# Performance work log

Measured on AMD Instinct MI355X. Metric: run time of the kernel, lower is better.

## Reference

```python
import jax, jax.numpy as jnp
import numpy as np

NUM_HEADS = 16


def setup_inputs() -> dict:
    key = jax.random.key(0)
    k1, k2, k3, k4, k5 = jax.random.split(key, 5)
    B, N, E = 16, 8, 2048
    H = NUM_HEADS
    D = E // H
    KV = 4096
    return {
        "x": jax.random.normal(k1, (B, N, E), dtype=jnp.float32),
        "past_k": jax.random.normal(k2, (B, H, KV, D), dtype=jnp.float32),
        "past_v": jax.random.normal(k3, (B, H, KV, D), dtype=jnp.float32),
        "W_qkv": jax.random.normal(k4, (3 * E, E), dtype=jnp.float32) * (E ** -0.5),
        "W_out": jax.random.normal(k5, (E, E), dtype=jnp.float32) * (E ** -0.5),
    }


def reference(x, past_k, past_v, W_qkv, W_out):
    B, N, E = x.shape
    H = NUM_HEADS
    D = E // H
    # fused QKV projection: [B, N, 3E]
    qkv = jnp.einsum("bne,fe->bnf", x, W_qkv)
    q, k_new, v_new = jnp.split(qkv, 3, axis=-1)
    # '... n (h d) -> ... h n d'
    to_heads = lambda t: t.reshape(B, N, H, D).swapaxes(1, 2)
    q, k_new, v_new = to_heads(q), to_heads(k_new), to_heads(v_new)
    # KV cache append along seq dim
    k = jnp.concatenate([past_k, k_new], axis=-2)  # [B, H, KV+N, D]
    v = jnp.concatenate([past_v, v_new], axis=-2)
    # SDPA (eval mode -> is_causal=False)
    scale = D ** -0.5
    scores = jnp.einsum("bhqd,bhkd->bhqk", q, k) * scale
    attn = jax.nn.softmax(scores, axis=-1)
    out = jnp.einsum("bhqk,bhkd->bhqd", attn, v)  # [B, H, N, D]
    # '... h n d -> ... n (h d)'
    out = out.swapaxes(1, 2).reshape(B, N, E)
    out = jnp.einsum("bne,fe->bnf", out, W_out)
    return (out, k, v)
```

## Files before the change

### kernel.cpp

```cpp
#include <hip/hip_runtime.h>
#include <cstddef>
#include <cstdint>

#define B_ 16
#define H_ 16
#define NQ 8
#define D_ 128
#define E_ 2048
#define F3 6144
#define KVP 4096
#define KVT 4104
#define SCALE 0.08838834764831843f
#define NCHUNK 8
#define CHUNK 512
#define SUBR 32
#define NSUB 16
#define PARTSZ 1040

typedef float f32x4_t __attribute__((ext_vector_type(4)));

__device__ __forceinline__ void nt_store4(float* p, float4 v) {
  f32x4_t w;
  w.x = v.x; w.y = v.y; w.z = v.z; w.w = v.w;
  __builtin_nontemporal_store(w, reinterpret_cast<f32x4_t*>(p));
}

template <int BM, int BN, int SPLITK>
__global__ __launch_bounds__(256) void gemm_xwt(const float* __restrict__ X,
                                                const float* __restrict__ W,
                                                float* __restrict__ C,
                                                int K, int Fdim) {
  constexpr int BK = 32;
  constexpr int RM = BM / 16;
  constexpr int RN = BN / 16;
  __shared__ float xs[BK][BM + 4];
  __shared__ float wss[BK][BN + 4];
  const int t = threadIdx.x;
  const int tm = t >> 4, tn = t & 15;
  const int m0 = blockIdx.y * BM, f0 = blockIdx.x * BN;
  const int kbeg = (SPLITK > 1) ? blockIdx.z * (K / SPLITK) : 0;
  const int kend = (SPLITK > 1) ? kbeg + K / SPLITK : K;
  if (SPLITK > 1) C += (size_t)blockIdx.z * 128 * Fdim;
  float acc[RM][RN];
#pragma unroll
  for (int i = 0; i < RM; ++i)
#pragma unroll
    for (int j = 0; j < RN; ++j) acc[i][j] = 0.f;

  for (int kk = kbeg; kk < kend; kk += BK) {
#pragma unroll
    for (int i = 0; i < (BM * BK) / 1024; ++i) {
      int j = t + i * 256;
      int r = j >> 3;
      int c = (j & 7) << 2;
      float4 v = *reinterpret_cast<const float4*>(&X[(size_t)(m0 + r) * K + kk + c]);
      xs[c + 0][r] = v.x; xs[c + 1][r] = v.y; xs[c + 2][r] = v.z; xs[c + 3][r] = v.w;
    }
#pragma unroll
    for (int i = 0; i < (BN * BK) / 1024; ++i) {
      int j = t + i * 256;
      int r = j >> 3;
      int c = (j & 7) << 2;
      float4 v = *reinterpret_cast<const float4*>(&W[(size_t)(f0 + r) * K + kk + c]);
      wss[c + 0][r] = v.x; wss[c + 1][r] = v.y; wss[c + 2][r] = v.z; wss[c + 3][r] = v.w;
    }
    __syncthreads();
#pragma unroll
    for (int k = 0; k < BK; ++k) {
      float xv[RM], wv[RN];
      if constexpr (RM == 4) {
        *reinterpret_cast<float4*>(xv) = *reinterpret_cast<const float4*>(&xs[k][tm * 4]);
      } else {
        *reinterpret_cast<float2*>(xv) = *reinterpret_cast<const float2*>(&xs[k][tm * 2]);
      }
      if constexpr (RN == 4) {
        *reinterpret_cast<float4*>(wv) = *reinterpret_cast<const float4*>(&wss[k][tn * 4]);
      } else {
        *reinterpret_cast<float2*>(wv) = *reinterpret_cast<const float2*>(&wss[k][tn * 2]);
      }
#pragma unroll
      for (int i = 0; i < RM; ++i)
#pragma unroll
        for (int j = 0; j < RN; ++j) acc[i][j] += xv[i] * wv[j];
    }
    __syncthreads();
  }
#pragma unroll
  for (int i = 0; i < RM; ++i) {
    float* cp = &C[(size_t)(m0 + tm * RM + i) * Fdim + f0 + tn * RN];
    if constexpr (RN == 4) {
      *reinterpret_cast<float4*>(cp) = make_float4(acc[i][0], acc[i][1], acc[i][2], acc[i][3]);
    } else {
      *reinterpret_cast<float2*>(cp) = make_float2(acc[i][0], acc[i][1]);
    }
  }
}

__global__ __launch_bounds__(256) void add2(const float* __restrict__ a,
                                            const float* __restrict__ b,
                                            float* __restrict__ o) {
  int i = blockIdx.x * 256 + threadIdx.x;
  float4 va = reinterpret_cast<const float4*>(a)[i];
  float4 vb = reinterpret_cast<const float4*>(b)[i];
  reinterpret_cast<float4*>(o)[i] =
      make_float4(va.x + vb.x, va.y + vb.y, va.z + vb.z, va.w + vb.w);
}

__global__ __launch_bounds__(256) void attn_partial(
    const float* __restrict__ past_k, const float* __restrict__ past_v,
    const float* __restrict__ qkv_a, const float* __restrict__ qkv_b,
    float* __restrict__ out_k, float* __restrict__ out_v,
    float* __restrict__ part) {
  const int t = threadIdx.x;
  const int c = blockIdx.x, h = blockIdx.y, b = blockIdx.z;
  const int bh = b * H_ + h;
  const int g = t & 31, rg = t >> 5;

  __shared__ float red[4096];
  __shared__ float f_lds[NQ];
  __shared__ float m_lds[2][NQ], l_lds[2][NQ];
  float* s_lds = red;
  float* p_lds = red + 288;

  float4 qreg[NQ];
#pragma unroll
  for (int qi = 0; qi < NQ; ++qi) {
    const size_t qoff = (size_t)(b * NQ + qi) * F3 + h * D_ + g * 4;
    float4 q0 = *reinterpret_cast<const float4*>(&qkv_a[qoff]);
    if (qkv_b) {
      float4 q1 = *reinterpret_cast<const float4*>(&qkv_b[qoff]);
      q0.x += q1.x; q0.y += q1.y; q0.z += q1.z; q0.w += q1.w;
    }
    qreg[qi] = q0;
  }

  if (t < NQ) { m_lds[0][t] = -1e30f; l_lds[0][t] = 0.f; }

  const float* gk = past_k + ((size_t)bh * KVP + (size_t)c * CHUNK) * D_;
  const float* gv = past_v + ((size_t)bh * KVP + (size_t)c * CHUNK) * D_;
  float* ok = out_k + ((size_t)bh * KVT + (size_t)c * CHUNK) * D_;
  float* ov = out_v + ((size_t)bh * KVT + (size_t)c * CHUNK) * D_;

  float4 acc[NQ];
#pragma unroll
  for (int qi = 0; qi < NQ; ++qi) acc[qi] = make_float4(0.f, 0.f, 0.f, 0.f);

  const int b0 = g & 1, b1 = (g >> 1) & 1, b2 = (g >> 2) & 1;
  const int qsel = 4 * b0 + 2 * b1 + b2;

  auto loadf = [&](float4 (&kf)[4], float4 (&vf)[4], int sub) {
    const size_t off = (size_t)sub * SUBR * D_;
#pragma unroll
    for (int i = 0; i < 4; ++i) {
      const size_t ga = off + (size_t)(rg + 8 * i) * D_ + g * 4;
      kf[i] = *reinterpret_cast<const float4*>(&gk[ga]);
      vf[i] = *reinterpret_cast<const float4*>(&gv[ga]);
    }
  };

  auto bodyf = [&](float4 (&kf)[4], float4 (&vf)[4], float4 (&kfN)[4],
                   float4 (&vfN)[4], int sub, bool pf) {
    const int cur = sub & 1, nxt = cur ^ 1;
    const size_t off = (size_t)sub * SUBR * D_;
#pragma unroll
    for (int i = 0; i < 4; ++i) {
      const int r = rg + 8 * i;
      const size_t ga = off + (size_t)r * D_ + g * 4;
      nt_store4(&ok[ga], kf[i]);
      nt_store4(&ov[ga], vf[i]);
      float sp[NQ];
#pragma unroll
      for (int qi = 0; qi < NQ; ++qi)
        sp[qi] = kf[i].x * qreg[qi].x + kf[i].y * qreg[qi].y +
                 kf[i].z * qreg[qi].z + kf[i].w * qreg[qi].w;
      float v1[4];
#pragma unroll
      for (int j = 0; j < 4; ++j) {
        float x = b0 ? sp[j] : sp[j + 4];
        v1[j] = (b0 ? sp[j + 4] : sp[j]) + __shfl_xor(x, 1);
      }
      float v2[2];
#pragma unroll
      for (int j = 0; j < 2; ++j) {
        float x = b1 ? v1[j] : v1[j + 2];
        v2[j] = (b1 ? v1[j + 2] : v1[j]) + __shfl_xor(x, 2);
      }
      float v3;
      {
        float x = b2 ? v2[0] : v2[1];
        v3 = (b2 ? v2[1] : v2[0]) + __shfl_xor(x, 4);
      }
      v3 += __shfl_xor(v3, 8);
      v3 += __shfl_xor(v3, 16);
      if (g < 8) s_lds[r * 9 + qsel] = v3;
    }
    __syncthreads();

    {
      const int srow = t & 31, sqi = t >> 5;
      float s = s_lds[srow * 9 + sqi] * SCALE;
      float cmax = s;
#pragma unroll
      for (int o = 16; o > 0; o >>= 1) cmax = fmaxf(cmax, __shfl_xor(cmax, o));
      float mo = m_lds[cur][sqi];
      float mn = fmaxf(mo, cmax);
      float p = __expf(s - mn);
      float psum = p;
#pragma unroll
      for (int o = 16; o > 0; o >>= 1) psum += __shfl_xor(psum, o);
      p_lds[srow * 8 + sqi] = p;
      if (srow == 0) {
        float f = __expf(mo - mn);
        f_lds[sqi] = f;
        m_lds[nxt][sqi] = mn;
        l_lds[nxt][sqi] = l_lds[cur][sqi] * f + psum;
      }
    }
    __syncthreads();

    if (pf) loadf(kfN, vfN, sub + 1);

    {
      float4 f0 = *reinterpret_cast<const float4*>(&f_lds[0]);
      float4 f1 = *reinterpret_cast<const float4*>(&f_lds[4]);
      acc[0].x *= f0.x; acc[0].y *= f0.x; acc[0].z *= f0.x; acc[0].w *= f0.x;
      acc[1].x *= f0.y; acc[1].y *= f0.y; acc[1].z *= f0.y; acc[1].w *= f0.y;
      acc[2].x *= f0.z; acc[2].y *= f0.z; acc[2].z *= f0.z; acc[2].w *= f0.z;
      acc[3].x *= f0.w; acc[3].y *= f0.w; acc[3].z *= f0.w; acc[3].w *= f0.w;
      acc[4].x *= f1.x; acc[4].y *= f1.x; acc[4].z *= f1.x; acc[4].w *= f1.x;
      acc[5].x *= f1.y; acc[5].y *= f1.y; acc[5].z *= f1.y; acc[5].w *= f1.y;
      acc[6].x *= f1.z; acc[6].y *= f1.z; acc[6].z *= f1.z; acc[6].w *= f1.z;
      acc[7].x *= f1.w; acc[7].y *= f1.w; acc[7].z *= f1.w; acc[7].w *= f1.w;
#pragma unroll
      for (int i = 0; i < 4; ++i) {
        const int r = rg + 8 * i;
        float4 pa = *reinterpret_cast<const float4*>(&p_lds[r * 8]);
        float4 pc = *reinterpret_cast<const float4*>(&p_lds[r * 8 + 4]);
        acc[0].x += pa.x * vf[i].x; acc[0].y += pa.x * vf[i].y; acc[0].z += pa.x * vf[i].z; acc[0].w += pa.x * vf[i].w;
        acc[1].x += pa.y * vf[i].x; acc[1].y += pa.y * vf[i].y; acc[1].z += pa.y * vf[i].z; acc[1].w += pa.y * vf[i].w;
        acc[2].x += pa.z * vf[i].x; acc[2].y += pa.z * vf[i].y; acc[2].z += pa.z * vf[i].z; acc[2].w += pa.z * vf[i].w;
        acc[3].x += pa.w * vf[i].x; acc[3].y += pa.w * vf[i].y; acc[3].z += pa.w * vf[i].z; acc[3].w += pa.w * vf[i].w;
        acc[4].x += pc.x * vf[i].x; acc[4].y += pc.x * vf[i].y; acc[4].z += pc.x * vf[i].z; acc[4].w += pc.x * vf[i].w;
        acc[5].x += pc.y * vf[i].x; acc[5].y += pc.y * vf[i].y; acc[5].z += pc.y * vf[i].z; acc[5].w += pc.y * vf[i].w;
        acc[6].x += pc.z * vf[i].x; acc[6].y += pc.z * vf[i].y; acc[6].z += pc.z * vf[i].z; acc[6].w += pc.z * vf[i].w;
        acc[7].x += pc.w * vf[i].x; acc[7].y += pc.w * vf[i].y; acc[7].z += pc.w * vf[i].z; acc[7].w += pc.w * vf[i].w;
      }
    }
  };

  __syncthreads();

  float4 kfA[4], vfA[4], kfB[4], vfB[4];
  loadf(kfA, vfA, 0);
  for (int sub = 0; sub < NSUB; sub += 2) {
    bodyf(kfA, vfA, kfB, vfB, sub, true);
    bodyf(kfB, vfB, kfA, vfA, sub + 1, sub + 2 < NSUB);
  }

  __syncthreads();

#pragma unroll
  for (int half = 4; half >= 1; half >>= 1) {
    if (rg >= half && rg < 2 * half) {
#pragma unroll
      for (int qi = 0; qi < NQ; ++qi)
        *reinterpret_cast<float4*>(&red[(rg - half) * 1024 + qi * 128 + g * 4]) = acc[qi];
    }
    __syncthreads();
    if (rg < half) {
#pragma unroll
      for (int qi = 0; qi < NQ; ++qi) {
        float4 o = *reinterpret_cast<const float4*>(&red[rg * 1024 + qi * 128 + g * 4]);
        acc[qi].x += o.x; acc[qi].y += o.y; acc[qi].z += o.z; acc[qi].w += o.w;
      }
    }
    __syncthreads();
  }

  float* pb = part + ((size_t)bh * NCHUNK + c) * PARTSZ;
  if (t < NQ) { pb[t] = m_lds[0][t]; pb[8 + t] = l_lds[0][t]; }
  if (rg == 0) {
#pragma unroll
    for (int qi = 0; qi < NQ; ++qi)
      *reinterpret_cast<float4*>(&pb[16 + qi * 128 + g * 4]) = acc[qi];
  }
}

__global__ __launch_bounds__(256) void attn_combine(
    const float* __restrict__ qkv_a, const float* __restrict__ qkv_b,
    const float* __restrict__ part, float* __restrict__ out_k,
    float* __restrict__ out_v, float* __restrict__ attn) {
  const int t = threadIdx.x;
  const int h = blockIdx.x, b = blockIdx.y;
  const int bh = b * H_ + h;
  __shared__ float q_lds[NQ * 132];
  __shared__ float kn_lds[NQ * 132];
  __shared__ float vn_lds[NQ * 132];
  __shared__ float p9[NQ * 12];
  __shared__ float m9_lds[NQ], s9_lds[NQ];
  {
    int n = t >> 5, g = t & 31;
    const size_t soff = (size_t)(b * NQ + n) * F3 + h * D_ + g * 4;
    float4 qv = *reinterpret_cast<const float4*>(&qkv_a[soff]);
    float4 kv = *reinterpret_cast<const float4*>(&qkv_a[soff + E_]);
    float4 vv = *reinterpret_cast<const float4*>(&qkv_a[soff + 2 * E_]);
    if (qkv_b) {
      float4 q1 = *reinterpret_cast<const float4*>(&qkv_b[soff]);
      float4 k1 = *reinterpret_cast<const float4*>(&qkv_b[soff + E_]);
      float4 v1 = *reinterpret_cast<const float4*>(&qkv_b[soff + 2 * E_]);
      qv.x += q1.x; qv.y += q1.y; qv.z += q1.z; qv.w += q1.w;
      kv.x += k1.x; kv.y += k1.y; kv.z += k1.z; kv.w += k1.w;
      vv.x += v1.x; vv.y += v1.y; vv.z += v1.z; vv.w += v1.w;
    }
    *reinterpret_cast<float4*>(&q_lds[n * 132 + g * 4]) = qv;
    *reinterpret_cast<float4*>(&kn_lds[n * 132 + g * 4]) = kv;
    *reinterpret_cast<float4*>(&vn_lds[n * 132 + g * 4]) = vv;
    *reinterpret_cast<float4*>(&out_k[((size_t)bh * KVT + KVP + n) * D_ + g * 4]) = kv;
    *reinterpret_cast<float4*>(&out_v[((size_t)bh * KVT + KVP + n) * D_ + g * 4]) = vv;
  }
  __syncthreads();
  if (t < 64) {
    int nq = t >> 3, nk = t & 7;
    float s = 0.f;
#pragma unroll
    for (int g = 0; g < 32; ++g) {
      float4 qv = *reinterpret_cast<const float4*>(&q_lds[nq * 132 + g * 4]);
      float4 kv = *reinterpret_cast<const float4*>(&kn_lds[nk * 132 + g * 4]);
      s += qv.x * kv.x + qv.y * kv.y + qv.z * kv.z + qv.w * kv.w;
    }
    s *= SCALE;
    float mx = s;
#pragma unroll
    for (int o = 4; o > 0; o >>= 1) mx = fmaxf(mx, __shfl_xor(mx, o));
    float p = __expf(s - mx);
    float sm = p;
#pragma unroll
    for (int o = 4; o > 0; o >>= 1) sm += __shfl_xor(sm, o);
    p9[nk * 12 + nq] = p;
    if (nk == 0) { m9_lds[nq] = mx; s9_lds[nq] = sm; }
  }
  __syncthreads();
  const int qg = t >> 7, dcol = t & 127;
  const float* pb = part + (size_t)bh * NCHUNK * PARTSZ;
#pragma unroll
  for (int jq = 0; jq < 4; ++jq) {
    int qi = qg * 4 + jq;
    float M = m9_lds[qi];
#pragma unroll
    for (int c = 0; c < NCHUNK; ++c) M = fmaxf(M, pb[(size_t)c * PARTSZ + qi]);
    float num = 0.f, den = 0.f;
#pragma unroll
    for (int c = 0; c < NCHUNK; ++c) {
      const float* pc = pb + (size_t)c * PARTSZ;
      float wgt = __expf(pc[qi] - M);
      den += wgt * pc[8 + qi];
      num += wgt * pc[16 + (size_t)qi * D_ + dcol];
    }
    float acc9 = 0.f;
#pragma unroll
    for (int r = 0; r < NQ; ++r) acc9 += p9[r * 12 + qi] * vn_lds[r * 132 + dcol];
    float w9 = __expf(m9_lds[qi] - M);
    num += w9 * acc9;
    den += w9 * s9_lds[qi];
    attn[((size_t)(b * NQ + qi)) * E_ + h * D_ + dcol] = num / den;
  }
}

extern "C" void kernel_launch(void* const* d_in, const int* in_sizes, int n_in,
                              void* d_out, int out_size, void* d_ws, size_t ws_size,
                              hipStream_t stream) {
  const float* x      = (const float*)d_in[0];
  const float* past_k = (const float*)d_in[1];
  const float* past_v = (const float*)d_in[2];
  const float* W_qkv  = (const float*)d_in[3];
  const float* W_out  = (const float*)d_in[4];

  float* out   = (float*)d_out;
  float* out_k = out + (size_t)B_ * NQ * E_;
  float* out_v = out_k + (size_t)B_ * H_ * KVT * D_;

  const size_t QKV_N  = (size_t)B_ * NQ * F3;
  const size_t PART_N = (size_t)B_ * H_ * NCHUNK * PARTSZ;
  const size_t ATTN_N = (size_t)B_ * NQ * E_;
  const size_t need2  = (2 * QKV_N + PART_N + 3 * ATTN_N) * sizeof(float);

  float* ws = (float*)d_ws;
  const bool split2 = ws_size >= need2;

  float* pq0  = ws;
  float* pq1  = split2 ? ws + QKV_N : nullptr;
  float* part = ws + (split2 ? 2 : 1) * QKV_N;
  float* attn = part + PART_N;
  float* po0  = attn + ATTN_N;

  if (split2) {
    gemm_xwt<64, 64, 2><<<dim3(F3 / 64, 2, 2), 256, 0, stream>>>(x, W_qkv, pq0, E_, F3);
  } else {
    gemm_xwt<64, 64, 1><<<dim3(F3 / 64, 2), 256, 0, stream>>>(x, W_qkv, pq0, E_, F3);
  }
  attn_partial<<<dim3(NCHUNK, H_, B_), 256, 0, stream>>>(past_k, past_v, pq0, pq1,
                                                         out_k, out_v, part);
  attn_combine<<<dim3(H_, B_), 256, 0, stream>>>(pq0, pq1, part, out_k, out_v, attn);
  if (split2) {
    gemm_xwt<64, 64, 2><<<dim3(E_ / 64, 2, 2), 256, 0, stream>>>(attn, W_out, po0, E_, E_);
    add2<<<dim3(ATTN_N / 1024), 256, 0, stream>>>(po0, po0 + ATTN_N, out);
  } else {
    gemm_xwt<64, 64, 1><<<dim3(E_ / 64, 2), 256, 0, stream>>>(attn, W_out, out, E_, E_);
  }
}
```

Before: 568.0 us.

## Give each wave its own KV slice with wave-local online softmax

Restructures attn_partial so each of the 4 waves owns 128 contiguous KV rows and keeps its own running max and sum in registers. Per-wave LDS scratch with an lgkmcnt fence replaces the block-wide __syncthreads barriers. The waves' partial results are merged at the end with a log-sum-exp rescale. Non-temporal stores become ordinary stores, and K/V prefetch is issued one step earlier. The cost is a more complex final combine and reliance on intra-wave LDS ordering without a barrier.

```diff
diff --git a/kernel.cpp b/kernel.cpp
--- a/kernel.cpp
+++ b/kernel.cpp
@@ -13,17 +13,9 @@
 #define SCALE 0.08838834764831843f
 #define NCHUNK 8
 #define CHUNK 512
-#define SUBR 32
-#define NSUB 16
 #define PARTSZ 1040
 
-typedef float f32x4_t __attribute__((ext_vector_type(4)));
-
-__device__ __forceinline__ void nt_store4(float* p, float4 v) {
-  f32x4_t w;
-  w.x = v.x; w.y = v.y; w.z = v.z; w.w = v.w;
-  __builtin_nontemporal_store(w, reinterpret_cast<f32x4_t*>(p));
-}
+#define WAVE_LDS_FENCE() asm volatile("s_waitcnt lgkmcnt(0)" ::: "memory")
 
 template <int BM, int BN, int SPLITK>
 __global__ __launch_bounds__(256) void gemm_xwt(const float* __restrict__ X,
@@ -114,13 +106,15 @@
   const int t = threadIdx.x;
   const int c = blockIdx.x, h = blockIdx.y, b = blockIdx.z;
   const int bh = b * H_ + h;
-  const int g = t & 31, rg = t >> 5;
+  const int l = t & 63, w = t >> 6;
+  const int g = l & 31, half = l >> 5;
 
   __shared__ float red[4096];
-  __shared__ float f_lds[NQ];
-  __shared__ float m_lds[2][NQ], l_lds[2][NQ];
-  float* s_lds = red;
-  float* p_lds = red + 288;
+  __shared__ float scratch[4][160];
+  __shared__ float mw_lds[32], lw_lds[32];
+  float* s_w = scratch[w];
+  float* p_w = scratch[w] + 72;
+  float* f_w = scratch[w] + 136;
 
   float4 qreg[NQ];
 #pragma unroll
@@ -134,8 +128,7 @@
     qreg[qi] = q0;
   }
 
-  if (t < NQ) { m_lds[0][t] = -1e30f; l_lds[0][t] = 0.f; }
-
+  const int wbase = w * 128;
   const float* gk = past_k + ((size_t)bh * KVP + (size_t)c * CHUNK) * D_;
   const float* gv = past_v + ((size_t)bh * KVP + (size_t)c * CHUNK) * D_;
   float* ok = out_k + ((size_t)bh * KVT + (size_t)c * CHUNK) * D_;
@@ -144,46 +137,44 @@
   float4 acc[NQ];
 #pragma unroll
   for (int qi = 0; qi < NQ; ++qi) acc[qi] = make_float4(0.f, 0.f, 0.f, 0.f);
+  float m_run = -1e30f, l_run = 0.f;
 
   const int b0 = g & 1, b1 = (g >> 1) & 1, b2 = (g >> 2) & 1;
   const int qsel = 4 * b0 + 2 * b1 + b2;
-
-  auto loadf = [&](float4 (&kf)[4], float4 (&vf)[4], int sub) {
-    const size_t off = (size_t)sub * SUBR * D_;
-#pragma unroll
-    for (int i = 0; i < 4; ++i) {
-      const size_t ga = off + (size_t)(rg + 8 * i) * D_ + g * 4;
-      kf[i] = *reinterpret_cast<const float4*>(&gk[ga]);
-      vf[i] = *reinterpret_cast<const float4*>(&gv[ga]);
+  const int srow = l & 7, sqi = l >> 3;
+
+  auto loadf = [&](float4 (&kf)[4], float4 (&vf)[4], int it) {
+#pragma unroll
+    for (int j = 0; j < 4; ++j) {
+      const size_t ga = (size_t)(wbase + it * 8 + half + 2 * j) * D_ + g * 4;
+      kf[j] = *reinterpret_cast<const float4*>(&gk[ga]);
+      vf[j] = *reinterpret_cast<const float4*>(&gv[ga]);
     }
   };
 
-  auto bodyf = [&](float4 (&kf)[4], float4 (&vf)[4], float4 (&kfN)[4],
-                   float4 (&vfN)[4], int sub, bool pf) {
-    const int cur = sub & 1, nxt = cur ^ 1;
-    const size_t off = (size_t)sub * SUBR * D_;
-#pragma unroll
-    for (int i = 0; i < 4; ++i) {
-      const int r = rg + 8 * i;
-      const size_t ga = off + (size_t)r * D_ + g * 4;
-      nt_store4(&ok[ga], kf[i]);
-      nt_store4(&ov[ga], vf[i]);
+  auto bodyf = [&](float4 (&kf)[4], float4 (&vf)[4], int it) {
+#pragma unroll
+    for (int j = 0; j < 4; ++j) {
+      const int r = half + 2 * j;
+      const size_t ga = (size_t)(wbase + it * 8 + r) * D_ + g * 4;
+      *reinterpret_cast<float4*>(&ok[ga]) = kf[j];
+      *reinterpret_cast<float4*>(&ov[ga]) = vf[j];
       float sp[NQ];
 #pragma unroll
       for (int qi = 0; qi < NQ; ++qi)
-        sp[qi] = kf[i].x * qreg[qi].x + kf[i].y * qreg[qi].y +
-                 kf[i].z * qreg[qi].z + kf[i].w * qreg[qi].w;
+        sp[qi] = kf[j].x * qreg[qi].x + kf[j].y * qreg[qi].y +
+                 kf[j].z * qreg[qi].z + kf[j].w * qreg[qi].w;
       float v1[4];
 #pragma unroll
-      for (int j = 0; j < 4; ++j) {
-        float x = b0 ? sp[j] : sp[j + 4];
-        v1[j] = (b0 ? sp[j + 4] : sp[j]) + __shfl_xor(x, 1);
+      for (int jj = 0; jj < 4; ++jj) {
+        float x = b0 ? sp[jj] : sp[jj + 4];
+        v1[jj] = (b0 ? sp[jj + 4] : sp[jj]) + __shfl_xor(x, 1);
       }
       float v2[2];
 #pragma unroll
-      for (int j = 0; j < 2; ++j) {
-        float x = b1 ? v1[j] : v1[j + 2];
-        v2[j] = (b1 ? v1[j + 2] : v1[j]) + __shfl_xor(x, 2);
+      for (int jj = 0; jj < 2; ++jj) {
+        float x = b1 ? v1[jj] : v1[jj + 2];
+        v2[jj] = (b1 ? v1[jj + 2] : v1[jj]) + __shfl_xor(x, 2);
       }
       float v3;
       {
@@ -192,37 +183,33 @@
       }
       v3 += __shfl_xor(v3, 8);
       v3 += __shfl_xor(v3, 16);
-      if (g < 8) s_lds[r * 9 + qsel] = v3;
-    }
-    __syncthreads();
+      if (g < 8) s_w[r * 9 + qsel] = v3;
+    }
+    WAVE_LDS_FENCE();
 
     {
-      const int srow = t & 31, sqi = t >> 5;
-      float s = s_lds[srow * 9 + sqi] * SCALE;
+      float s = s_w[srow * 9 + sqi] * SCALE;
       float cmax = s;
-#pragma unroll
-      for (int o = 16; o > 0; o >>= 1) cmax = fmaxf(cmax, __shfl_xor(cmax, o));
-      float mo = m_lds[cur][sqi];
-      float mn = fmaxf(mo, cmax);
+      cmax = fmaxf(cmax, __shfl_xor(cmax, 1));
+      cmax = fmaxf(cmax, __shfl_xor(cmax, 2));
+      cmax = fmaxf(cmax, __shfl_xor(cmax, 4));
+      float mn = fmaxf(m_run, cmax);
       float p = __expf(s - mn);
-      float psum = p;
-#pragma unroll
-      for (int o = 16; o > 0; o >>= 1) psum += __shfl_xor(psum, o);
-      p_lds[srow * 8 + sqi] = p;
-      if (srow == 0) {
-        float f = __expf(mo - mn);
-        f_lds[sqi] = f;
-        m_lds[nxt][sqi] = mn;
-        l_lds[nxt][sqi] = l_lds[cur][sqi] * f + psum;
-      }
-    }
-    __syncthreads();
-
-    if (pf) loadf(kfN, vfN, sub + 1);
+      float ps = p;
+      ps += __shfl_xor(ps, 1);
+      ps += __shfl_xor(ps, 2);
+      ps += __shfl_xor(ps, 4);
+      float f = __expf(m_run - mn);
+      p_w[srow * 8 + sqi] = p;
+      if (srow == 0) f_w[sqi] = f;
+      l_run = l_run * f + ps;
+      m_run = mn;
+    }
+    WAVE_LDS_FENCE();
 
     {
-      float4 f0 = *reinterpret_cast<const float4*>(&f_lds[0]);
-      float4 f1 = *reinterpret_cast<const float4*>(&f_lds[4]);
+      float4 f0 = *reinterpret_cast<const float4*>(&f_w[0]);
+      float4 f1 = *reinterpret_cast<const float4*>(&f_w[4]);
       acc[0].x *= f0.x; acc[0].y *= f0.x; acc[0].z *= f0.x; acc[0].w *= f0.x;
       acc[1].x *= f0.y; acc[1].y *= f0.y; acc[1].z *= f0.y; acc[1].w *= f0.y;
       acc[2].x *= f0.z; acc[2].y *= f0.z; acc[2].z *= f0.z; acc[2].w *= f0.z;
@@ -232,57 +219,65 @@
       acc[6].x *= f1.z; acc[6].y *= f1.z; acc[6].z *= f1.z; acc[6].w *= f1.z;
       acc[7].x *= f1.w; acc[7].y *= f1.w; acc[7].z *= f1.w; acc[7].w *= f1.w;
 #pragma unroll
-      for (int i = 0; i < 4; ++i) {
-        const int r = rg + 8 * i;
-        float4 pa = *reinterpret_cast<const float4*>(&p_lds[r * 8]);
-        float4 pc = *reinterpret_cast<const float4*>(&p_lds[r * 8 + 4]);
-        acc[0].x += pa.x * vf[i].x; acc[0].y += pa.x * vf[i].y; acc[0].z += pa.x * vf[i].z; acc[0].w += pa.x * vf[i].w;
-        acc[1].x += pa.y * vf[i].x; acc[1].y += pa.y * vf[i].y; acc[1].z += pa.y * vf[i].z; acc[1].w += pa.y * vf[i].w;
-        acc[2].x += pa.z * vf[i].x; acc[2].y += pa.z * vf[i].y; acc[2].z += pa.z * vf[i].z; acc[2].w += pa.z * vf[i].w;
-        acc[3].x += pa.w * vf[i].x; acc[3].y += pa.w * vf[i].y; acc[3].z += pa.w * vf[i].z; acc[3].w += pa.w * vf[i].w;
-        acc[4].x += pc.x * vf[i].x; acc[4].y += pc.x * vf[i].y; acc[4].z += pc.x * vf[i].z; acc[4].w += pc.x * vf[i].w;
-        acc[5].x += pc.y * vf[i].x; acc[5].y += pc.y * vf[i].y; acc[5].z += pc.y * vf[i].z; acc[5].w += pc.y * vf[i].w;
-        acc[6].x += pc.z * vf[i].x; acc[6].y += pc.z * vf[i].y; acc[6].z += pc.z * vf[i].z; acc[6].w += pc.z * vf[i].w;
-        acc[7].x += pc.w * vf[i].x; acc[7].y += pc.w * vf[i].y; acc[7].z += pc.w * vf[i].z; acc[7].w += pc.w * vf[i].w;
+      for (int j = 0; j < 4; ++j) {
+        const int r = half + 2 * j;
+        float4 pa = *reinterpret_cast<const float4*>(&p_w[r * 8]);
+        float4 pc = *reinterpret_cast<const float4*>(&p_w[r * 8 + 4]);
+        acc[0].x += pa.x * vf[j].x; acc[0].y += pa.x * vf[j].y; acc[0].z += pa.x * vf[j].z; acc[0].w += pa.x * vf[j].w;
+        acc[1].x += pa.y * vf[j].x; acc[1].y += pa.y * vf[j].y; acc[1].z += pa.y * vf[j].z; acc[1].w += pa.y * vf[j].w;
+        acc[2].x += pa.z * vf[j].x; acc[2].y += pa.z * vf[j].y; acc[2].z += pa.z * vf[j].z; acc[2].w += pa.z * vf[j].w;
+        acc[3].x += pa.w * vf[j].x; acc[3].y += pa.w * vf[j].y; acc[3].z += pa.w * vf[j].z; acc[3].w += pa.w * vf[j].w;
+        acc[4].x += pc.x * vf[j].x; acc[4].y += pc.x * vf[j].y; acc[4].z += pc.x * vf[j].z; acc[4].w += pc.x * vf[j].w;
+        acc[5].x += pc.y * vf[j].x; acc[5].y += pc.y * vf[j].y; acc[5].z += pc.y * vf[j].z; acc[5].w += pc.y * vf[j].w;
+        acc[6].x += pc.z * vf[j].x; acc[6].y += pc.z * vf[j].y; acc[6].z += pc.z * vf[j].z; acc[6].w += pc.z * vf[j].w;
+        acc[7].x += pc.w * vf[j].x; acc[7].y += pc.w * vf[j].y; acc[7].z += pc.w * vf[j].z; acc[7].w += pc.w * vf[j].w;
       }
     }
   };
 
+  float4 kA[4], vA[4], kB[4], vB[4];
+  loadf(kA, vA, 0);
+  for (int it = 0; it < 16; it += 2) {
+    if (it + 1 < 16) loadf(kB, vB, it + 1);
+    bodyf(kA, vA, it);
+    if (it + 2 < 16) loadf(kA, vA, it + 2);
+    bodyf(kB, vB, it + 1);
+  }
+
+#pragma unroll
+  for (int qi = 0; qi < NQ; ++qi) {
+    acc[qi].x += __shfl_xor(acc[qi].x, 32);
+    acc[qi].y += __shfl_xor(acc[qi].y, 32);
+    acc[qi].z += __shfl_xor(acc[qi].z, 32);
+    acc[qi].w += __shfl_xor(acc[qi].w, 32);
+  }
+
+  if (srow == 0) { mw_lds[w * 8 + sqi] = m_run; lw_lds[w * 8 + sqi] = l_run; }
+  if (half == 0) {
+#pragma unroll
+    for (int qi = 0; qi < NQ; ++qi)
+      *reinterpret_cast<float4*>(&red[w * 1024 + qi * 128 + g * 4]) = acc[qi];
+  }
   __syncthreads();
 
-  float4 kfA[4], vfA[4], kfB[4], vfB[4];
-  loadf(kfA, vfA, 0);
-  for (int sub = 0; sub < NSUB; sub += 2) {
-    bodyf(kfA, vfA, kfB, vfB, sub, true);
-    bodyf(kfB, vfB, kfA, vfA, sub + 1, sub + 2 < NSUB);
-  }
-
-  __syncthreads();
-
-#pragma unroll
-  for (int half = 4; half >= 1; half >>= 1) {
-    if (rg >= half && rg < 2 * half) {
-#pragma unroll
-      for (int qi = 0; qi < NQ; ++qi)
-        *reinterpret_cast<float4*>(&red[(rg - half) * 1024 + qi * 128 + g * 4]) = acc[qi];
-    }
-    __syncthreads();
-    if (rg < half) {
-#pragma unroll
-      for (int qi = 0; qi < NQ; ++qi) {
-        float4 o = *reinterpret_cast<const float4*>(&red[rg * 1024 + qi * 128 + g * 4]);
-        acc[qi].x += o.x; acc[qi].y += o.y; acc[qi].z += o.z; acc[qi].w += o.w;
-      }
-    }
-    __syncthreads();
-  }
-
-  float* pb = part + ((size_t)bh * NCHUNK + c) * PARTSZ;
-  if (t < NQ) { pb[t] = m_lds[0][t]; pb[8 + t] = l_lds[0][t]; }
-  if (rg == 0) {
-#pragma unroll
-    for (int qi = 0; qi < NQ; ++qi)
-      *reinterpret_cast<float4*>(&pb[16 + qi * 128 + g * 4]) = acc[qi];
+  {
+    const int col4 = t & 31, qi = (t >> 5) & 7;
+    float M = mw_lds[qi];
+    M = fmaxf(M, mw_lds[8 + qi]);
+    M = fmaxf(M, mw_lds[16 + qi]);
+    M = fmaxf(M, mw_lds[24 + qi]);
+    float den = 0.f;
+    float4 num = make_float4(0.f, 0.f, 0.f, 0.f);
+#pragma unroll
+    for (int ww = 0; ww < 4; ++ww) {
+      float wt = __expf(mw_lds[ww * 8 + qi] - M);
+      den += wt * lw_lds[ww * 8 + qi];
+      float4 a = *reinterpret_cast<const float4*>(&red[ww * 1024 + qi * 128 + col4 * 4]);
+      num.x += wt * a.x; num.y += wt * a.y; num.z += wt * a.z; num.w += wt * a.w;
+    }
+    float* pb = part + ((size_t)bh * NCHUNK + c) * PARTSZ;
+    *reinterpret_cast<float4*>(&pb[16 + qi * 128 + col4 * 4]) = num;
+    if (col4 == 0) { pb[qi] = M; pb[8 + qi] = den; }
   }
 }
 
```

Measured after the change: 565.5 us. No clear change (-0.4%).
